# Optimization experiments

Measured on AMD Instinct MI355X. Metric: run time of the kernel, lower is better.

## Reference

```python
import jax, jax.numpy as jnp
import numpy as np

SHIFT = 1  # module picks random +/-1 at init; fixed to +1 for determinism


def setup_inputs() -> dict:
    key = jax.random.key(0)
    k1, k2, k3 = jax.random.split(key, 3)
    return {
        "x": jax.random.normal(k1, (1, 24, 56, 56), dtype=jnp.float32),
        "W0": jax.random.normal(k2, (48, 9), dtype=jnp.float32),   # weights[0]
        "W1": jax.random.normal(k3, (12, 7, 9), dtype=jnp.float32),  # weights[1]
    }


def reference(x, W0, W1):
    # x -> (o=2, j=12, n=56, m=56); n is folded into unfold channels,
    # the sliding window (k=7, pad=3) runs over m.
    a = x.reshape(2, 12, 56, 56)
    ap = jnp.pad(a, ((0, 0), (0, 0), (0, 0), (3, 3)))  # pad the windowed axis
    idx = jnp.arange(7)[:, None] + jnp.arange(56)[None, :]  # (k, m) gather indices
    t3 = ap[:, :, :, idx]  # (o, j, n, k, m) == torch (1,2,12,56,7,56) with l=1 dropped
    # einsum('lojnkm, jki -> lonmi')
    t4 = jnp.einsum('ojnkm,jki->onmi', t3, W1)  # (2, 56, 56, 9)
    # einsum('knmli, ji -> knjml') with t4 axes renamed -> (o, p, n, m)
    t5 = jnp.einsum('onmi,pi->opnm', t4, W0)    # (2, 48, 56, 56)
    y = t5.reshape(1, 96, 56, 56)
    return jnp.roll(y, SHIFT, axis=2)
```

## Files before the change

### kernel.cpp

```cpp
#include <hip/hip_runtime.h>
#include <hip/hip_bf16.h>


__global__ __launch_bounds__(256) void fused_shiftconv_v2(
    const float* __restrict__ x,
    const float* __restrict__ W0,
    const float* __restrict__ W1,
    float* __restrict__ out)
{
    __shared__ __align__(16) float sA[12][64];
    __shared__ __align__(16) float sW1[756];
    __shared__ __align__(16) float sW0[432];
    __shared__ __align__(16) float sPart[4][9][60];
    __shared__ __align__(16) float sT4t[9][60];

    const int tid = threadIdx.x;
    const int o = blockIdx.x / 56;
    const int n = blockIdx.x % 56;

    {
        const float4* W1v = (const float4*)W1;
        float4* s1 = (float4*)sW1;
        for (int idx = tid; idx < 189; idx += 256) s1[idx] = W1v[idx];
        const float4* W0v = (const float4*)W0;
        float4* s0 = (float4*)sW0;
        for (int idx = tid; idx < 108; idx += 256) s0[idx] = W0v[idx];
    }

    for (int idx = tid; idx < 12 * 64; idx += 256) {
        const int j = idx >> 6, mm = idx & 63;
        const int ms = mm - 3;
        float v = 0.0f;
        if (ms >= 0 && ms < 56)
            v = x[((o * 12 + j) * 56 + n) * 56 + ms];
        sA[j][mm] = v;
    }
    __syncthreads();

    {
        const int wave = tid >> 6, lane = tid & 63;
        if (lane < 56) {
            const int m = lane;
            float acc[9];
#pragma unroll
            for (int i = 0; i < 9; ++i) acc[i] = 0.0f;
#pragma unroll
            for (int jj = 0; jj < 3; ++jj) {
                const int j = wave * 3 + jj;
#pragma unroll
                for (int k = 0; k < 7; ++k) {
                    const float v = sA[j][m + k];
                    const float* w = &sW1[(j * 7 + k) * 9];
#pragma unroll
                    for (int i = 0; i < 9; ++i) acc[i] += v * w[i];
                }
            }
#pragma unroll
            for (int i = 0; i < 9; ++i) sPart[wave][i][m] = acc[i];
        }
    }
    __syncthreads();

    for (int idx = tid; idx < 504; idx += 256) {
        const int i = idx / 56, m = idx % 56;
        sT4t[i][m] = sPart[0][i][m] + sPart[1][i][m]
                   + sPart[2][i][m] + sPart[3][i][m];
    }
    __syncthreads();

    const int n_out = (n + 1) % 56;
    for (int v4 = tid; v4 < 672; v4 += 256) {
        const int p = v4 / 14;
        const int m0 = (v4 % 14) * 4;
        const float* w = &sW0[p * 9];
        float4 acc = {0.0f, 0.0f, 0.0f, 0.0f};
#pragma unroll
        for (int i = 0; i < 9; ++i) {
            const float4 t = *(const float4*)&sT4t[i][m0];
            const float wi = w[i];
            acc.x += wi * t.x; acc.y += wi * t.y;
            acc.z += wi * t.z; acc.w += wi * t.w;
        }
        *(float4*)&out[((o * 48 + p) * 56 + n_out) * 56 + m0] = acc;
    }
}

extern "C" void kernel_launch(void* const* d_in, const int* in_sizes, int n_in,
                              void* d_out, int out_size, void* d_ws, size_t ws_size,
                              hipStream_t stream) {
    const float* x  = (const float*)d_in[0];
    const float* W0 = (const float*)d_in[1];
    const float* W1 = (const float*)d_in[2];
    float* out = (float*)d_out;

    fused_shiftconv_v2<<<dim3(112), dim3(256), 0, stream>>>(x, W0, W1, out);
}
```

Measured before the change: 60.43 us.

## Split output channels across two blocks and vectorize shared-memory loads

The grid doubles to 224 blocks, and each block writes half of the 48 output channels so more CUs are busy. The cost is that each block recomputes the same W1 stage. The input row is loaded with float4 accesses plus explicit zero padding instead of a scalar guarded loop. W1 is repacked into 12-wide padded rows so the inner loop can read weights with float4 loads. The partial-sum reduction also uses float4. Together these aim to cut load latency and instruction count in a small, latency-bound kernel.

```diff
diff --git a/kernel.cpp b/kernel.cpp
--- a/kernel.cpp
+++ b/kernel.cpp
@@ -1,40 +1,45 @@
 #include <hip/hip_runtime.h>
-#include <hip/hip_bf16.h>
 
 
-__global__ __launch_bounds__(256) void fused_shiftconv_v2(
+__global__ __launch_bounds__(256) void fused_shiftconv_v3(
     const float* __restrict__ x,
     const float* __restrict__ W0,
     const float* __restrict__ W1,
     float* __restrict__ out)
 {
     __shared__ __align__(16) float sA[12][64];
-    __shared__ __align__(16) float sW1[756];
+    __shared__ __align__(16) float sW1p[84][12];
     __shared__ __align__(16) float sW0[432];
     __shared__ __align__(16) float sPart[4][9][60];
     __shared__ __align__(16) float sT4t[9][60];
 
     const int tid = threadIdx.x;
-    const int o = blockIdx.x / 56;
-    const int n = blockIdx.x % 56;
+    const int b   = blockIdx.x;
+    const int h   = b & 1;
+    const int on  = b >> 1;
+    const int o   = on / 56;
+    const int n   = on % 56;
 
-    {
-        const float4* W1v = (const float4*)W1;
-        float4* s1 = (float4*)sW1;
-        for (int idx = tid; idx < 189; idx += 256) s1[idx] = W1v[idx];
-        const float4* W0v = (const float4*)W0;
-        float4* s0 = (float4*)sW0;
-        for (int idx = tid; idx < 108; idx += 256) s0[idx] = W0v[idx];
+    if (tid < 168) {
+        const int j = tid / 14, q = tid % 14;
+        *(float4*)&sA[j][4 + 4*q] =
+            *(const float4*)(x + (((o*12 + j)*56 + n)*56 + 4*q));
+    } else if (tid < 192) {
+        const int t = tid - 168;
+        *(float4*)&sA[t >> 1][(t & 1) ? 60 : 0] =
+            make_float4(0.f, 0.f, 0.f, 0.f);
     }
-
-    for (int idx = tid; idx < 12 * 64; idx += 256) {
-        const int j = idx >> 6, mm = idx & 63;
-        const int ms = mm - 3;
-        float v = 0.0f;
-        if (ms >= 0 && ms < 56)
-            v = x[((o * 12 + j) * 56 + n) * 56 + ms];
-        sA[j][mm] = v;
+    if (tid < 189) {
+        const float4 v = ((const float4*)W1)[tid];
+        const float vv[4] = {v.x, v.y, v.z, v.w};
+#pragma unroll
+        for (int c = 0; c < 4; ++c) {
+            const int e  = tid*4 + c;
+            const int jk = e / 9;
+            ((float*)sW1p)[jk*12 + (e - jk*9)] = vv[c];
+        }
     }
+    if (tid < 108) ((float4*)sW0)[tid] = ((const float4*)W0)[tid];
     __syncthreads();
 
     {
@@ -46,13 +51,19 @@
             for (int i = 0; i < 9; ++i) acc[i] = 0.0f;
 #pragma unroll
             for (int jj = 0; jj < 3; ++jj) {
-                const int j = wave * 3 + jj;
+                const int j = wave*3 + jj;
 #pragma unroll
                 for (int k = 0; k < 7; ++k) {
-                    const float v = sA[j][m + k];
-                    const float* w = &sW1[(j * 7 + k) * 9];
-#pragma unroll
-                    for (int i = 0; i < 9; ++i) acc[i] += v * w[i];
+                    const float v  = sA[j][m + k + 1];
+                    const float* wp = &sW1p[j*7 + k][0];
+                    const float4 wa = *(const float4*)(wp);
+                    const float4 wb = *(const float4*)(wp + 4);
+                    const float  w8 = wp[8];
+                    acc[0] += v*wa.x; acc[1] += v*wa.y;
+                    acc[2] += v*wa.z; acc[3] += v*wa.w;
+                    acc[4] += v*wb.x; acc[5] += v*wb.y;
+                    acc[6] += v*wb.z; acc[7] += v*wb.w;
+                    acc[8] += v*w8;
                 }
             }
 #pragma unroll
@@ -61,27 +72,36 @@
     }
     __syncthreads();
 
-    for (int idx = tid; idx < 504; idx += 256) {
-        const int i = idx / 56, m = idx % 56;
-        sT4t[i][m] = sPart[0][i][m] + sPart[1][i][m]
-                   + sPart[2][i][m] + sPart[3][i][m];
+    if (tid < 126) {
+        const int i = tid / 14, m0 = (tid % 14) * 4;
+        const float4 s0 = *(const float4*)&sPart[0][i][m0];
+        const float4 s1 = *(const float4*)&sPart[1][i][m0];
+        const float4 s2 = *(const float4*)&sPart[2][i][m0];
+        const float4 s3 = *(const float4*)&sPart[3][i][m0];
+        float4 r;
+        r.x = (s0.x + s1.x) + (s2.x + s3.x);
+        r.y = (s0.y + s1.y) + (s2.y + s3.y);
+        r.z = (s0.z + s1.z) + (s2.z + s3.z);
+        r.w = (s0.w + s1.w) + (s2.w + s3.w);
+        *(float4*)&sT4t[i][m0] = r;
     }
     __syncthreads();
 
     const int n_out = (n + 1) % 56;
-    for (int v4 = tid; v4 < 672; v4 += 256) {
-        const int p = v4 / 14;
+    for (int v4 = tid; v4 < 336; v4 += 256) {
+        const int pl = v4 / 14;
         const int m0 = (v4 % 14) * 4;
+        const int p  = h*24 + pl;
         const float* w = &sW0[p * 9];
-        float4 acc = {0.0f, 0.0f, 0.0f, 0.0f};
+        float4 acc = make_float4(0.0f, 0.0f, 0.0f, 0.0f);
 #pragma unroll
         for (int i = 0; i < 9; ++i) {
             const float4 t = *(const float4*)&sT4t[i][m0];
             const float wi = w[i];
-            acc.x += wi * t.x; acc.y += wi * t.y;
-            acc.z += wi * t.z; acc.w += wi * t.w;
+            acc.x += wi*t.x; acc.y += wi*t.y;
+            acc.z += wi*t.z; acc.w += wi*t.w;
         }
-        *(float4*)&out[((o * 48 + p) * 56 + n_out) * 56 + m0] = acc;
+        *(float4*)&out[((o*48 + p)*56 + n_out)*56 + m0] = acc;
     }
 }
 
@@ -93,5 +113,5 @@
     const float* W1 = (const float*)d_in[2];
     float* out = (float*)d_out;
 
-    fused_shiftconv_v2<<<dim3(112), dim3(256), 0, stream>>>(x, W0, W1, out);
+    fused_shiftconv_v3<<<dim3(224), dim3(256), 0, stream>>>(x, W0, W1, out);
 }
```

After: 59.21 us. 2.0% less time.
